# Performance work log

Measured on AMD Instinct MI355X. Metric: run time of the kernel, lower is better.

Reference implementation:

```python
import jax, jax.numpy as jnp
import numpy as np

HIDDEN = 1024
N_HEAD = 16
LN_EPS = 1e-5


def _layernorm(x, g, b):
    m = jnp.mean(x, axis=-1, keepdims=True)
    v = jnp.var(x, axis=-1, keepdims=True)
    return (x - m) * jax.lax.rsqrt(v + LN_EPS) * g + b


def setup_inputs() -> dict:
    key = jax.random.key(0)
    ks = jax.random.split(key, 16)
    H = HIDDEN
    s = 0.02
    d = dict(
        x=jax.random.normal(ks[0], (4, 1024, H), jnp.float32),
        Wq=jax.random.normal(ks[1], (H, H), jnp.float32) * s,
        bq=jnp.zeros((H,), jnp.float32),
        Wk=jax.random.normal(ks[2], (H, H), jnp.float32) * s,
        bk=jnp.zeros((H,), jnp.float32),
        Wv=jax.random.normal(ks[3], (H, H), jnp.float32) * s,
        bv=jnp.zeros((H,), jnp.float32),
        Wo=jax.random.normal(ks[4], (H, H), jnp.float32) * s,
        bo=jnp.zeros((H,), jnp.float32),
        g1=jax.random.normal(ks[5], (H,), jnp.float32) * s,
        b1=jnp.zeros((H,), jnp.float32),
        W1=jax.random.normal(ks[6], (H, 4 * H), jnp.float32) * s,
        c1=jnp.zeros((4 * H,), jnp.float32),
        W2=jax.random.normal(ks[7], (4 * H, H), jnp.float32) * s,
        c2=jnp.zeros((H,), jnp.float32),
        g2=jax.random.normal(ks[8], (H,), jnp.float32) * s,
        b2=jnp.zeros((H,), jnp.float32),
    )
    return d


def reference(x, Wq, bq, Wk, bk, Wv, bv, Wo, bo, g1, b1, W1, c1, W2, c2, g2, b2):
    N, T, Hd = x.shape
    Hh = N_HEAD
    D = Hd // Hh
    # faithful to torch code: .view(N, H, T, D) is a raw reshape, no transpose
    q = (x @ Wq + bq).reshape(N, Hh, T, D)
    k = (x @ Wk + bk).reshape(N, Hh, T, D)
    v = (x @ Wv + bv).reshape(N, Hh, T, D)
    scores = jnp.einsum('nhtd,nhsd->nhts', q, k) / jnp.sqrt(jnp.float32(Hd))
    # faithful: softmax over dim=1 (the head axis)
    attn = jax.nn.softmax(scores, axis=1)
    o = jnp.einsum('nhts,nhsd->nhtd', attn, v).reshape(N, T, Hd)
    o = o @ Wo + bo
    x1 = _layernorm(o + x, g1, b1)
    ff = jax.nn.gelu(x1 @ W1 + c1, approximate=False) @ W2 + c2
    return _layernorm(ff + x1, g2, b2)
```

## Files before the change

kernel.cpp:

```cpp
#include <hip/hip_runtime.h>
#include <cstdint>
#include <cstddef>

#define EPI_QKV  0
#define EPI_F32  2
#define EPI_GELU 3
#define EPI_PART 4

typedef __attribute__((ext_vector_type(8))) short bfrag8;
typedef __attribute__((ext_vector_type(4))) float facc4;

struct PtrQuad { unsigned short* p[4]; };

__device__ __forceinline__ unsigned short f2b(float x) {
  unsigned int u = __builtin_bit_cast(unsigned int, x);
  u += 0x7FFFu + ((u >> 16) & 1u);
  return (unsigned short)(u >> 16);
}
__device__ __forceinline__ float b2f(unsigned short u) {
  unsigned int x = ((unsigned int)u) << 16;
  return __builtin_bit_cast(float, x);
}

__device__ __forceinline__ void gl2lds16(const unsigned short* g, unsigned short* l) {
  __builtin_amdgcn_global_load_lds(
      (const __attribute__((address_space(1))) unsigned int*)g,
      (__attribute__((address_space(3))) unsigned int*)l, 16, 0, 0);
}

__global__ __launch_bounds__(256)
void cvt_bf16_kernel(const float* __restrict__ in, unsigned short* __restrict__ out, int n4) {
  const int i = blockIdx.x * 256 + threadIdx.x;
  if (i < n4) {
    const float4 v = ((const float4*)in)[i];
    ushort4 u;
    u.x = f2b(v.x); u.y = f2b(v.y); u.z = f2b(v.z); u.w = f2b(v.w);
    ((ushort4*)out)[i] = u;
  }
}

__global__ __launch_bounds__(256)
void transpose_cvt(const float* __restrict__ in, unsigned short* __restrict__ out,
                   int K, int N) {
  __shared__ float tile[32][33];
  const int n0 = blockIdx.x * 32;
  const int k0 = blockIdx.y * 32;
  const int tx = threadIdx.x & 31, ty = threadIdx.x >> 5;
#pragma unroll
  for (int i = 0; i < 32; i += 8)
    tile[ty + i][tx] = in[(size_t)(k0 + ty + i) * N + n0 + tx];
  __syncthreads();
#pragma unroll
  for (int i = 0; i < 32; i += 8)
    out[(size_t)(n0 + ty + i) * K + k0 + tx] = f2b(tile[tx][ty + i]);
}

template<int EPI>
__global__ __launch_bounds__(256, 2)
void gemm_bt(const unsigned short* __restrict__ A,
             const unsigned short* __restrict__ Bt,
             const float* __restrict__ bias,
             const float* __restrict__ bias2,
             const float* __restrict__ bias3,
             void* __restrict__ out, PtrQuad pq,
             int M, int N, int K, int ldk) {
  __shared__ unsigned short sA[128 * 32];
  __shared__ unsigned short sB[128 * 32];
  const int tid  = threadIdx.x;
  const int lane = tid & 63;
  const int wave = tid >> 6;
  const int l15  = lane & 15, l4 = lane >> 4;
  const int wr = wave >> 1, wc = wave & 1;
  const long row0 = (long)blockIdx.y * 128;
  const long col0 = (long)blockIdx.x * 128;
  const long k0   = (long)blockIdx.z * K;

  facc4 acc[4][4];
#pragma unroll
  for (int i = 0; i < 4; i++)
#pragma unroll
    for (int j = 0; j < 4; j++) acc[i][j] = (facc4)0.f;

  const int srow = tid >> 2;
  const int scol = (tid & 3) * 8;
  const unsigned short* Ap0 = A  + (row0 + srow) * (long)ldk + k0 + scol;
  const unsigned short* Ap1 = Ap0 + 64 * (long)ldk;
  const unsigned short* Bp0 = Bt + (col0 + srow) * (long)ldk + k0 + scol;
  const unsigned short* Bp1 = Bp0 + 64 * (long)ldk;
  const int wbase = (tid & ~63) * 8;
  unsigned short* sA0 = &sA[wbase];
  unsigned short* sA1 = &sA[2048 + wbase];
  unsigned short* sB0 = &sB[wbase];
  unsigned short* sB1 = &sB[2048 + wbase];

  const int aoff = (wr * 64 + l15) * 32 + l4 * 8;
  const int boff = (wc * 64 + l15) * 32 + l4 * 8;

  for (int kt = 0; kt < K; kt += 32) {
    gl2lds16(Ap0 + kt, sA0);
    gl2lds16(Ap1 + kt, sA1);
    gl2lds16(Bp0 + kt, sB0);
    gl2lds16(Bp1 + kt, sB1);
    __syncthreads();
    bfrag8 af[4], bf[4];
#pragma unroll
    for (int i = 0; i < 4; i++) af[i] = *(const bfrag8*)&sA[aoff + i * 512];
#pragma unroll
    for (int j = 0; j < 4; j++) bf[j] = *(const bfrag8*)&sB[boff + j * 512];
#pragma unroll
    for (int i = 0; i < 4; i++)
#pragma unroll
      for (int j = 0; j < 4; j++)
        acc[i][j] = __builtin_amdgcn_mfma_f32_16x16x32_bf16(af[i], bf[j], acc[i][j], 0, 0, 0);
    __syncthreads();
  }

#pragma unroll
  for (int i = 0; i < 4; i++) {
    const long m0 = row0 + wr * 64 + i * 16 + l4 * 4;
#pragma unroll
    for (int j = 0; j < 4; j++) {
      const long c = col0 + wc * 64 + j * 16 + l15;
      if constexpr (EPI == EPI_QKV) {
        const long which = c >> 10;
        const long cl = c & 1023;
        unsigned short* oq = (unsigned short*)out;
        if (which == 0) {
          const float bj = bias[cl];
#pragma unroll
          for (int r = 0; r < 4; r++)
            oq[(m0 + r) * 1024 + cl] = f2b((acc[i][j][r] + bj) * 0.03125f);
        } else if (which == 1) {
          const float bj = bias2[cl];
#pragma unroll
          for (int r = 0; r < 4; r++)
            (oq + 4194304)[(m0 + r) * 1024 + cl] = f2b(acc[i][j][r] + bj);
        } else {
          const float bj = bias3[cl];
          const long cc = cl >> 6, d = cl & 63;
#pragma unroll
          for (int r = 0; r < 4; r++) {
            const long m = m0 + r;
            const long nbb = m >> 10, rr = m & 1023;
            const long h = rr >> 6, rhi = rr & 63;
            const long s = rhi * 16 + cc;
            (oq + 8388608)[((nbb * 16 + h) * 64 + d) * 1024 + s] = f2b(acc[i][j][r] + bj);
          }
        }
      } else if constexpr (EPI == EPI_F32) {
        const float bj = bias[c];
        float* of = (float*)out;
#pragma unroll
        for (int r = 0; r < 4; r++) of[(m0 + r) * (long)N + c] = acc[i][j][r] + bj;
      } else if constexpr (EPI == EPI_PART) {
        unsigned short* ob = pq.p[blockIdx.z];
#pragma unroll
        for (int r = 0; r < 4; r++) ob[(m0 + r) * (long)N + c] = f2b(acc[i][j][r]);
      } else {
        const float bj = bias[c];
        unsigned short* ob = (unsigned short*)out;
#pragma unroll
        for (int r = 0; r < 4; r++) {
          const float t = acc[i][j][r] + bj;
          ob[(m0 + r) * (long)N + c] = f2b(0.5f * t * (1.f + erff(t * 0.70710678f)));
        }
      }
    }
  }
}

__global__ __launch_bounds__(512, 1)
void attn_kernel(const unsigned short* __restrict__ Qb,
                 const unsigned short* __restrict__ Kb,
                 const unsigned short* __restrict__ Vt,
                 PtrQuad APQ) {
  const int id = blockIdx.x;
  const int combo = id & 15;
  const int nb = combo & 3;
  const int sp = combo >> 2;
  const int tile = id >> 4;
  const int tid = threadIdx.x, lane = tid & 63;
  const int w = __builtin_amdgcn_readfirstlane(tid >> 6);
  const int l15 = lane & 15, l4 = lane >> 4;
  const int t0 = tile * 32;
  const int sbase = sp * 256;
  const int h0 = w * 2;

  __shared__ __align__(16) float Ds[8][32][68];
  __shared__ __align__(16) float Dt[32][68];

  const size_t bb = ((size_t)(nb * 16)) << 16;
  const unsigned short* qB = Qb + bb;
  const unsigned short* kB = Kb + bb;
  const unsigned short* vB = Vt + bb;

  bfrag8 qf[2][2][2];
#pragma unroll
  for (int hh = 0; hh < 2; hh++)
#pragma unroll
    for (int ts = 0; ts < 2; ts++)
#pragma unroll
      for (int dh = 0; dh < 2; dh++)
        qf[hh][ts][dh] = *(const bfrag8*)(qB + ((size_t)(h0 + hh) << 16)
            + (size_t)(t0 + ts * 16 + l15) * 64 + dh * 32 + l4 * 8);

  const int swz = (l15 & 7) << 4;
  char* pw = (char*)&Ds[w][0][0];
  const int pwrow = l15 * 128;
  const int ti1 = tid >> 4;
  const int si1 = (tid & 15) * 4;

  facc4 oacc[2][2][4];
#pragma unroll
  for (int hh = 0; hh < 2; hh++)
#pragma unroll
    for (int ts = 0; ts < 2; ts++)
#pragma unroll
      for (int nt = 0; nt < 4; nt++) oacc[hh][ts][nt] = (facc4)0.f;

  for (int it = 0; it < 4; ++it) {
    const int s0 = sbase + it * 64;
    bfrag8 kf[2][4][2];
#pragma unroll
    for (int hh = 0; hh < 2; hh++) {
      const unsigned short* kh_ = kB + ((size_t)(h0 + hh) << 16) + (size_t)l15 * 64 + l4 * 8;
#pragma unroll
      for (int ss = 0; ss < 4; ss++)
#pragma unroll
        for (int kh = 0; kh < 2; kh++)
          kf[hh][ss][kh] = *(const bfrag8*)(kh_ + (size_t)(s0 + ss * 16) * 64 + kh * 32);
    }
    facc4 sc[2][2][4];
#pragma unroll
    for (int hh = 0; hh < 2; hh++)
#pragma unroll
      for (int ts = 0; ts < 2; ts++)
#pragma unroll
        for (int ss = 0; ss < 4; ss++) {
          facc4 a = __builtin_amdgcn_mfma_f32_16x16x32_bf16(kf[hh][ss][0], qf[hh][ts][0],
                                                            (facc4)0.f, 0, 0, 0);
          sc[hh][ts][ss] = __builtin_amdgcn_mfma_f32_16x16x32_bf16(kf[hh][ss][1],
                                                                   qf[hh][ts][1], a, 0, 0, 0);
        }
    bfrag8 vf[2][2][4];
#pragma unroll
    for (int hh = 0; hh < 2; hh++) {
      const unsigned short* vh_ = vB + ((size_t)(h0 + hh) << 16) + (size_t)l15 * 1024 + s0 + l4 * 8;
#pragma unroll
      for (int sk = 0; sk < 2; sk++)
#pragma unroll
        for (int nt = 0; nt < 4; nt++)
          vf[hh][sk][nt] = *(const bfrag8*)(vh_ + (size_t)(nt * 16) * 1024 + sk * 32);
    }
    facc4 dacc[2][4];
#pragma unroll
    for (int ts = 0; ts < 2; ts++)
#pragma unroll
      for (int ss = 0; ss < 4; ss++) dacc[ts][ss] = (facc4)0.f;
#pragma unroll
    for (int hh = 0; hh < 2; hh++)
#pragma unroll
      for (int ts = 0; ts < 2; ts++)
#pragma unroll
        for (int ss = 0; ss < 4; ss++)
#pragma unroll
          for (int r = 0; r < 4; r++) {
            const float e = __expf(sc[hh][ts][ss][r]);
            sc[hh][ts][ss][r] = e;
            dacc[ts][ss][r] += e;
          }
#pragma unroll
    for (int ts = 0; ts < 2; ts++)
#pragma unroll
      for (int ss = 0; ss < 4; ss++)
        *(facc4*)&Ds[w][ts * 16 + l15][ss * 16 + l4 * 4] = dacc[ts][ss];
    __syncthreads();
    {
      facc4 s_ = *(const facc4*)&Ds[0][ti1][si1];
#pragma unroll
      for (int ww = 1; ww < 8; ww++) s_ += *(const facc4*)&Ds[ww][ti1][si1];
      *(facc4*)&Dt[ti1][si1] = s_;
    }
    __syncthreads();
    facc4 rt[2][4];
#pragma unroll
    for (int ts = 0; ts < 2; ts++)
#pragma unroll
      for (int ss = 0; ss < 4; ss++) {
        const facc4 d = *(const facc4*)&Dt[ts * 16 + l15][ss * 16 + l4 * 4];
#pragma unroll
        for (int r = 0; r < 4; r++) rt[ts][ss][r] = __builtin_amdgcn_rcpf(d[r]);
      }
#pragma unroll
    for (int hh = 0; hh < 2; hh++)
#pragma unroll
      for (int ts = 0; ts < 2; ts++) {
#pragma unroll
        for (int ss = 0; ss < 4; ss++) {
          const float p0 = sc[hh][ts][ss][0] * rt[ts][ss][0];
          const float p1 = sc[hh][ts][ss][1] * rt[ts][ss][1];
          const float p2 = sc[hh][ts][ss][2] * rt[ts][ss][2];
          const float p3 = sc[hh][ts][ss][3] * rt[ts][ss][3];
          uint2 pk;
          asm("v_cvt_pk_bf16_f32 %0, %1, %2" : "=v"(pk.x) : "v"(p0), "v"(p1));
          asm("v_cvt_pk_bf16_f32 %0, %1, %2" : "=v"(pk.y) : "v"(p2), "v"(p3));
          *(uint2*)(pw + pwrow + ((ss * 32 + l4 * 8) ^ swz)) = pk;
        }
        const bfrag8 a0 = *(const bfrag8*)(pw + pwrow + ((l4 * 16) ^ swz));
        const bfrag8 a1 = *(const bfrag8*)(pw + pwrow + ((64 + l4 * 16) ^ swz));
#pragma unroll
        for (int nt = 0; nt < 4; nt++) {
          oacc[hh][ts][nt] = __builtin_amdgcn_mfma_f32_16x16x32_bf16(a0, vf[hh][0][nt],
                                                                    oacc[hh][ts][nt], 0, 0, 0);
          oacc[hh][ts][nt] = __builtin_amdgcn_mfma_f32_16x16x32_bf16(a1, vf[hh][1][nt],
                                                                    oacc[hh][ts][nt], 0, 0, 0);
        }
      }
  }

  unsigned short* P = APQ.p[sp];
#pragma unroll
  for (int hh = 0; hh < 2; hh++) {
    const size_t hb = ((size_t)nb << 20) + ((size_t)(h0 + hh) << 16);
#pragma unroll
    for (int ts = 0; ts < 2; ts++)
#pragma unroll
      for (int nt = 0; nt < 4; nt++)
#pragma unroll
        for (int r = 0; r < 4; r++)
          P[hb + (size_t)(t0 + ts * 16 + l4 * 4 + r) * 64 + nt * 16 + l15] =
              f2b(oacc[hh][ts][nt][r]);
  }
}

__global__ __launch_bounds__(256)
void reduce_o4(PtrQuad pq, unsigned short* __restrict__ OB, int n4) {
  const int i = blockIdx.x * 256 + threadIdx.x;
  if (i < n4) {
    const ushort4 a = ((const ushort4*)pq.p[0])[i];
    const ushort4 b = ((const ushort4*)pq.p[1])[i];
    const ushort4 c = ((const ushort4*)pq.p[2])[i];
    const ushort4 d = ((const ushort4*)pq.p[3])[i];
    ushort4 u;
    u.x = f2b(b2f(a.x) + b2f(b.x) + b2f(c.x) + b2f(d.x));
    u.y = f2b(b2f(a.y) + b2f(b.y) + b2f(c.y) + b2f(d.y));
    u.z = f2b(b2f(a.z) + b2f(b.z) + b2f(c.z) + b2f(d.z));
    u.w = f2b(b2f(a.w) + b2f(b.w) + b2f(c.w) + b2f(d.w));
    ((ushort4*)OB)[i] = u;
  }
}

__global__ __launch_bounds__(256)
void ln_red(const unsigned short* __restrict__ P0, const unsigned short* __restrict__ P1,
            const unsigned short* __restrict__ P2, const unsigned short* __restrict__ P3,
            const float* __restrict__ bias, const float* __restrict__ resid,
            const float* __restrict__ g, const float* __restrict__ be,
            float* __restrict__ outf, unsigned short* __restrict__ outb) {
  const int row = blockIdx.x, tid = threadIdx.x;
  const size_t o4 = (size_t)row * 256 + tid;
  const ushort4 a = ((const ushort4*)P0)[o4];
  const ushort4 b = ((const ushort4*)P1)[o4];
  const ushort4 c = ((const ushort4*)P2)[o4];
  const ushort4 d = ((const ushort4*)P3)[o4];
  const float4 vb = ((const float4*)bias)[tid];
  const float4 vr = ((const float4*)resid)[o4];
  float t0 = b2f(a.x) + b2f(b.x) + b2f(c.x) + b2f(d.x) + vb.x + vr.x;
  float t1 = b2f(a.y) + b2f(b.y) + b2f(c.y) + b2f(d.y) + vb.y + vr.y;
  float t2 = b2f(a.z) + b2f(b.z) + b2f(c.z) + b2f(d.z) + vb.z + vr.z;
  float t3 = b2f(a.w) + b2f(b.w) + b2f(c.w) + b2f(d.w) + vb.w + vr.w;
  float s = t0 + t1 + t2 + t3;
  float q = t0 * t0 + t1 * t1 + t2 * t2 + t3 * t3;
#pragma unroll
  for (int off = 32; off > 0; off >>= 1) {
    s += __shfl_down(s, off, 64);
    q += __shfl_down(q, off, 64);
  }
  __shared__ float rs_[4], rq_[4];
  if ((tid & 63) == 0) { rs_[tid >> 6] = s; rq_[tid >> 6] = q; }
  __syncthreads();
  const float S = rs_[0] + rs_[1] + rs_[2] + rs_[3];
  const float Q = rq_[0] + rq_[1] + rq_[2] + rq_[3];
  const float mean = S * (1.f / 1024.f);
  const float var  = Q * (1.f / 1024.f) - mean * mean;
  const float rstd = rsqrtf(var + 1e-5f);
  const float4 vg  = ((const float4*)g)[tid];
  const float4 vbe = ((const float4*)be)[tid];
  float o0 = (t0 - mean) * rstd * vg.x + vbe.x;
  float o1 = (t1 - mean) * rstd * vg.y + vbe.y;
  float o2 = (t2 - mean) * rstd * vg.z + vbe.z;
  float o3 = (t3 - mean) * rstd * vg.w + vbe.w;
  ((float4*)(outf + (size_t)row * 1024))[tid] = make_float4(o0, o1, o2, o3);
  if (outb != nullptr) {
    ushort4 u;
    u.x = f2b(o0); u.y = f2b(o1); u.z = f2b(o2); u.w = f2b(o3);
    ((ushort4*)(outb + (size_t)row * 1024))[tid] = u;
  }
}

extern "C" void kernel_launch(void* const* d_in, const int* in_sizes, int n_in,
                              void* d_out, int out_size, void* d_ws, size_t ws_size,
                              hipStream_t stream) {
  const float* x  = (const float*)d_in[0];
  const float* Wq = (const float*)d_in[1];
  const float* bq = (const float*)d_in[2];
  const float* Wk = (const float*)d_in[3];
  const float* bk = (const float*)d_in[4];
  const float* Wv = (const float*)d_in[5];
  const float* bv = (const float*)d_in[6];
  const float* Wo = (const float*)d_in[7];
  const float* bo = (const float*)d_in[8];
  const float* g1 = (const float*)d_in[9];
  const float* b1 = (const float*)d_in[10];
  const float* W1 = (const float*)d_in[11];
  const float* c1 = (const float*)d_in[12];
  const float* W2 = (const float*)d_in[13];
  const float* c2 = (const float*)d_in[14];
  const float* g2 = (const float*)d_in[15];
  const float* b2 = (const float*)d_in[16];
  float* out = (float*)d_out;

  char* ws = (char*)d_ws;
  unsigned short* XB  = (unsigned short*)(ws);
  unsigned short* WQT = (unsigned short*)(ws + 8388608);
  unsigned short* WKT = (unsigned short*)(ws + 10485760);
  unsigned short* WVT = (unsigned short*)(ws + 12582912);
  unsigned short* WOT = (unsigned short*)(ws + 14680064);
  unsigned short* W1T = (unsigned short*)(ws + 16777216);
  unsigned short* W2T = (unsigned short*)(ws + 25165824);
  float*          X1  = (float*)(ws + 33554432);
  unsigned short* X1B = (unsigned short*)(ws + 50331648);
  char* RB = ws + 58720256;
  unsigned short* QB  = (unsigned short*)(RB);
  unsigned short* KB  = (unsigned short*)(RB + 8388608);
  unsigned short* VT  = (unsigned short*)(RB + 16777216);
  unsigned short* OB  = (unsigned short*)(RB + 25165824);
  unsigned short* H1B = (unsigned short*)(RB);
  unsigned short* AP0 = (unsigned short*)(RB + 33554432);
  unsigned short* AP1 = (unsigned short*)(RB + 41943040);
  unsigned short* AP2 = (unsigned short*)(ws + 33554432);
  unsigned short* AP3 = (unsigned short*)(ws + 41943040);
  PtrQuad APQ = { { AP0, AP1, AP2, AP3 } };
  PtrQuad OPQ = { { QB, KB, VT, XB } };
  PtrQuad FPQ = { { XB, X1B, (unsigned short*)(RB + 33554432),
                    (unsigned short*)(RB + 41943040) } };
  PtrQuad ZQ = { { nullptr, nullptr, nullptr, nullptr } };

  const dim3 tb(256);
  cvt_bf16_kernel<<<dim3(4096), tb, 0, stream>>>(x, XB, 1048576);
  transpose_cvt<<<dim3(32, 32),  tb, 0, stream>>>(Wq, WQT, 1024, 1024);
  transpose_cvt<<<dim3(32, 32),  tb, 0, stream>>>(Wk, WKT, 1024, 1024);
  transpose_cvt<<<dim3(32, 32),  tb, 0, stream>>>(Wv, WVT, 1024, 1024);
  transpose_cvt<<<dim3(32, 32),  tb, 0, stream>>>(Wo, WOT, 1024, 1024);
  transpose_cvt<<<dim3(128, 32), tb, 0, stream>>>(W1, W1T, 1024, 4096);
  transpose_cvt<<<dim3(32, 128), tb, 0, stream>>>(W2, W2T, 4096, 1024);
  gemm_bt<EPI_QKV><<<dim3(24, 32), tb, 0, stream>>>(XB, WQT, bq, bk, bv, (void*)QB, ZQ,
                                                    4096, 3072, 1024, 1024);
  attn_kernel<<<dim3(512), dim3(512), 0, stream>>>(QB, KB, VT, APQ);
  reduce_o4<<<dim3(4096), tb, 0, stream>>>(APQ, OB, 1048576);
  gemm_bt<EPI_PART><<<dim3(8, 32, 4), tb, 0, stream>>>(OB, WOT, nullptr, nullptr, nullptr,
                                                       nullptr, OPQ, 4096, 1024, 256, 1024);
  ln_red<<<dim3(4096), tb, 0, stream>>>(QB, KB, VT, XB, bo, x, g1, b1, X1, X1B);
  gemm_bt<EPI_GELU><<<dim3(32, 32), tb, 0, stream>>>(X1B, W1T, c1, nullptr, nullptr,
                                                     (void*)H1B, ZQ, 4096, 4096, 1024, 1024);
  gemm_bt<EPI_PART><<<dim3(8, 32, 4), tb, 0, stream>>>(H1B, W2T, nullptr, nullptr, nullptr,
                                                       nullptr, FPQ, 4096, 1024, 1024, 4096);
  ln_red<<<dim3(4096), tb, 0, stream>>>(FPQ.p[0], FPQ.p[1], FPQ.p[2], FPQ.p[3], c2, X1,
                                        g2, b2, out, (unsigned short*)nullptr);
}
```

Before: 421.8 us.

## Merge weight prep launches and move V transpose out of QKV epilogue

After: 399.3 us. 5.3% less time.

```diff
diff --git a/kernel.cpp b/kernel.cpp
--- a/kernel.cpp
+++ b/kernel.cpp
@@ -9,8 +9,10 @@
 
 typedef __attribute__((ext_vector_type(8))) short bfrag8;
 typedef __attribute__((ext_vector_type(4))) float facc4;
+typedef __attribute__((ext_vector_type(8))) unsigned short ush8;
 
 struct PtrQuad { unsigned short* p[4]; };
+struct Ptr4f  { const float* p[4]; };
 
 __device__ __forceinline__ unsigned short f2b(float x) {
   unsigned int u = __builtin_bit_cast(unsigned int, x);
@@ -28,24 +30,12 @@
       (__attribute__((address_space(3))) unsigned int*)l, 16, 0, 0);
 }
 
-__global__ __launch_bounds__(256)
-void cvt_bf16_kernel(const float* __restrict__ in, unsigned short* __restrict__ out, int n4) {
-  const int i = blockIdx.x * 256 + threadIdx.x;
-  if (i < n4) {
-    const float4 v = ((const float4*)in)[i];
-    ushort4 u;
-    u.x = f2b(v.x); u.y = f2b(v.y); u.z = f2b(v.z); u.w = f2b(v.w);
-    ((ushort4*)out)[i] = u;
-  }
-}
-
-__global__ __launch_bounds__(256)
-void transpose_cvt(const float* __restrict__ in, unsigned short* __restrict__ out,
-                   int K, int N) {
-  __shared__ float tile[32][33];
-  const int n0 = blockIdx.x * 32;
-  const int k0 = blockIdx.y * 32;
-  const int tx = threadIdx.x & 31, ty = threadIdx.x >> 5;
+__device__ __forceinline__ void tr_tile(const float* __restrict__ in,
+                                        unsigned short* __restrict__ out,
+                                        int K, int N, int bx, int by,
+                                        float (*tile)[33], int tid) {
+  const int n0 = bx * 32, k0 = by * 32;
+  const int tx = tid & 31, ty = tid >> 5;
 #pragma unroll
   for (int i = 0; i < 32; i += 8)
     tile[ty + i][tx] = in[(size_t)(k0 + ty + i) * N + n0 + tx];
@@ -53,6 +43,67 @@
 #pragma unroll
   for (int i = 0; i < 32; i += 8)
     out[(size_t)(n0 + ty + i) * K + k0 + tx] = f2b(tile[tx][ty + i]);
+}
+
+__global__ __launch_bounds__(256)
+void prep_kernel(const float* __restrict__ x, unsigned short* __restrict__ XB,
+                 Ptr4f Ws, PtrQuad WTs,
+                 const float* __restrict__ W1, unsigned short* __restrict__ W1T,
+                 const float* __restrict__ W2, unsigned short* __restrict__ W2T) {
+  __shared__ float tile[32][33];
+  int b = blockIdx.x;
+  const int tid = threadIdx.x;
+  if (b < 4096) {
+    const int i = b * 256 + tid;
+    const float4 v = ((const float4*)x)[i];
+    ushort4 u;
+    u.x = f2b(v.x); u.y = f2b(v.y); u.z = f2b(v.z); u.w = f2b(v.w);
+    ((ushort4*)XB)[i] = u;
+    return;
+  }
+  b -= 4096;
+  if (b < 4096) {
+    const int which = b >> 10, t = b & 1023;
+    tr_tile(Ws.p[which], WTs.p[which], 1024, 1024, t & 31, t >> 5, tile, tid);
+    return;
+  }
+  b -= 4096;
+  if (b < 4096) {
+    tr_tile(W1, W1T, 1024, 4096, b & 127, b >> 7, tile, tid);
+    return;
+  }
+  b -= 4096;
+  tr_tile(W2, W2T, 4096, 1024, b & 31, b >> 5, tile, tid);
+}
+
+__global__ __launch_bounds__(256)
+void transpose_v(const unsigned short* __restrict__ VR, unsigned short* __restrict__ VT) {
+  __shared__ __align__(16) unsigned short tile[8][16][72];
+  const int at = blockIdx.x;
+  const int hb = blockIdx.y;
+  const int nb = hb >> 4;
+  const int tid = threadIdx.x;
+  const size_t src = ((size_t)nb * 1024 + (size_t)(hb & 15) * 64 + (size_t)at * 8) * 1024;
+#pragma unroll
+  for (int p = 0; p < 4; p++) {
+    const int idx = p * 256 + tid;
+    const int a = idx >> 7, c8 = idx & 127;
+    *(ush8*)&tile[a][c8 >> 3][(c8 & 7) * 8] =
+        *(const ush8*)&VR[src + (size_t)a * 1024 + (size_t)c8 * 8];
+  }
+  __syncthreads();
+  const size_t dst = (size_t)hb * 65536 + (size_t)at * 128;
+#pragma unroll
+  for (int p = 0; p < 8; p++) {
+    const int idx = p * 256 + tid;
+    const int dd = idx >> 5, q = idx & 31;
+    ushort4 u;
+    u.x = tile[(q * 4 + 0) >> 4][(q * 4 + 0) & 15][dd];
+    u.y = tile[(q * 4 + 1) >> 4][(q * 4 + 1) & 15][dd];
+    u.z = tile[(q * 4 + 2) >> 4][(q * 4 + 2) & 15][dd];
+    u.w = tile[(q * 4 + 3) >> 4][(q * 4 + 3) & 15][dd];
+    *(ushort4*)&VT[dst + (size_t)dd * 1024 + (size_t)q * 4] = u;
+  }
 }
 
 template<int EPI>
@@ -137,15 +188,10 @@
             (oq + 4194304)[(m0 + r) * 1024 + cl] = f2b(acc[i][j][r] + bj);
         } else {
           const float bj = bias3[cl];
-          const long cc = cl >> 6, d = cl & 63;
-#pragma unroll
-          for (int r = 0; r < 4; r++) {
-            const long m = m0 + r;
-            const long nbb = m >> 10, rr = m & 1023;
-            const long h = rr >> 6, rhi = rr & 63;
-            const long s = rhi * 16 + cc;
-            (oq + 8388608)[((nbb * 16 + h) * 64 + d) * 1024 + s] = f2b(acc[i][j][r] + bj);
-          }
+          unsigned short* vr = pq.p[0];
+#pragma unroll
+          for (int r = 0; r < 4; r++)
+            vr[(m0 + r) * 1024 + cl] = f2b(acc[i][j][r] + bj);
         }
       } else if constexpr (EPI == EPI_F32) {
         const float bj = bias[c];
@@ -434,6 +480,7 @@
   unsigned short* KB  = (unsigned short*)(RB + 8388608);
   unsigned short* VT  = (unsigned short*)(RB + 16777216);
   unsigned short* OB  = (unsigned short*)(RB + 25165824);
+  unsigned short* VR  = OB;
   unsigned short* H1B = (unsigned short*)(RB);
   unsigned short* AP0 = (unsigned short*)(RB + 33554432);
   unsigned short* AP1 = (unsigned short*)(RB + 41943040);
@@ -443,18 +490,16 @@
   PtrQuad OPQ = { { QB, KB, VT, XB } };
   PtrQuad FPQ = { { XB, X1B, (unsigned short*)(RB + 33554432),
                     (unsigned short*)(RB + 41943040) } };
-  PtrQuad ZQ = { { nullptr, nullptr, nullptr, nullptr } };
+  PtrQuad VQ  = { { VR, nullptr, nullptr, nullptr } };
+  PtrQuad ZQ  = { { nullptr, nullptr, nullptr, nullptr } };
+  Ptr4f  Ws   = { { Wq, Wk, Wv, Wo } };
+  PtrQuad WTs = { { WQT, WKT, WVT, WOT } };
 
   const dim3 tb(256);
-  cvt_bf16_kernel<<<dim3(4096), tb, 0, stream>>>(x, XB, 1048576);
-  transpose_cvt<<<dim3(32, 32),  tb, 0, stream>>>(Wq, WQT, 1024, 1024);
-  transpose_cvt<<<dim3(32, 32),  tb, 0, stream>>>(Wk, WKT, 1024, 1024);
-  transpose_cvt<<<dim3(32, 32),  tb, 0, stream>>>(Wv, WVT, 1024, 1024);
-  transpose_cvt<<<dim3(32, 32),  tb, 0, stream>>>(Wo, WOT, 1024, 1024);
-  transpose_cvt<<<dim3(128, 32), tb, 0, stream>>>(W1, W1T, 1024, 4096);
-  transpose_cvt<<<dim3(32, 128), tb, 0, stream>>>(W2, W2T, 4096, 1024);
-  gemm_bt<EPI_QKV><<<dim3(24, 32), tb, 0, stream>>>(XB, WQT, bq, bk, bv, (void*)QB, ZQ,
+  prep_kernel<<<dim3(16384), tb, 0, stream>>>(x, XB, Ws, WTs, W1, W1T, W2, W2T);
+  gemm_bt<EPI_QKV><<<dim3(24, 32), tb, 0, stream>>>(XB, WQT, bq, bk, bv, (void*)QB, VQ,
                                                     4096, 3072, 1024, 1024);
+  transpose_v<<<dim3(8, 64), tb, 0, stream>>>(VR, VT);
   attn_kernel<<<dim3(512), dim3(512), 0, stream>>>(QB, KB, VT, APQ);
   reduce_o4<<<dim3(4096), tb, 0, stream>>>(APQ, OB, 1048576);
   gemm_bt<EPI_PART><<<dim3(8, 32, 4), tb, 0, stream>>>(OB, WOT, nullptr, nullptr, nullptr,
```
